# Optimization experiments

Measured on AMD Instinct MI355X. Metric: run time of the kernel, lower is better.

Reference implementation:

```python
import jax, jax.numpy as jnp
import numpy as np
from jax.scipy.special import gammaln

# sizes (see shape_source)
N_CELLS = 1024
N_GENES = 1000
N_LATENT = 50
NB_ENC = 16          # encoder histogram bins per gene
NB_DEC = 16          # decoder mixture components (sum(n_decoder_bins))
N_HID = 16           # encoder hidden dim
N_CUTS = 4_000_000
N_FRAGS = 2_000_000
N_TOTAL_CELLS = 10_000
N_TOTAL_CUTS = 50_000_000
BN_EPS = 1e-5


def _normal_logprob(x, loc, scale):
    z = (x - loc) / scale
    return -0.5 * z * z - jnp.log(scale) - 0.5 * jnp.log(2.0 * jnp.pi)


def setup_inputs() -> dict:
    key = jax.random.key(0)
    ks = jax.random.split(key, 20)
    cut_coordinates = jax.random.uniform(ks[0], (N_CUTS,), dtype=jnp.float32)
    cut_cell = jax.random.randint(ks[1], (N_CUTS,), 0, N_CELLS)
    cut_local_gene_ix = jax.random.randint(ks[2], (N_CUTS,), 0, N_GENES)
    cut_local_cellxgene_ix = cut_cell * N_GENES + cut_local_gene_ix
    local_cellxgene_ix = jax.random.randint(ks[3], (N_FRAGS,), 0, N_CELLS * N_GENES)
    genes_oi = jnp.arange(N_GENES)
    cells_oi = jnp.arange(N_CELLS)
    eps = jax.random.normal(ks[4], (N_CELLS, N_LATENT), dtype=jnp.float32)
    n_in = N_GENES * NB_ENC
    enc_W1 = jax.random.normal(ks[5], (n_in, N_HID)) * (1.0 / np.sqrt(n_in))
    enc_b1 = jnp.zeros((N_HID,))
    bn_gamma = jnp.ones((N_HID,))
    bn_beta = jnp.zeros((N_HID,))
    W_loc = jax.random.normal(ks[6], (N_HID, N_LATENT)) * (1.0 / np.sqrt(N_HID))
    b_loc = jnp.zeros((N_LATENT,))
    W_scale = jax.random.normal(ks[7], (N_HID, N_LATENT)) * (1.0 / np.sqrt(N_HID))
    b_scale = jnp.zeros((N_LATENT,))
    logit_weight = jax.random.normal(ks[8], (N_GENES, N_LATENT, NB_DEC)) * 0.05
    rho_weight = jax.random.normal(ks[9], (N_GENES, N_LATENT)) * 0.05
    baseline_heights = jax.random.normal(ks[10], (N_GENES, NB_DEC)) * 0.1
    libsize = jax.random.randint(ks[11], (N_TOTAL_CELLS,), 1000, 20000)
    rho_bias = jax.random.uniform(ks[12], (N_GENES,), minval=1e-4, maxval=1e-2)
    return dict(
        cut_coordinates=cut_coordinates, eps=eps,
        enc_W1=enc_W1, enc_b1=enc_b1, bn_gamma=bn_gamma, bn_beta=bn_beta,
        W_loc=W_loc, b_loc=b_loc, W_scale=W_scale, b_scale=b_scale,
        logit_weight=logit_weight, rho_weight=rho_weight,
        baseline_heights=baseline_heights, rho_bias=rho_bias,
        cut_local_cellxgene_ix=cut_local_cellxgene_ix,
        cut_local_gene_ix=cut_local_gene_ix,
        local_cellxgene_ix=local_cellxgene_ix,
        genes_oi=genes_oi, cells_oi=cells_oi, libsize=libsize,
    )


def reference(cut_coordinates, eps, enc_W1, enc_b1, bn_gamma, bn_beta,
              W_loc, b_loc, W_scale, b_scale, logit_weight, rho_weight,
              baseline_heights, rho_bias, cut_local_cellxgene_ix,
              cut_local_gene_ix, local_cellxgene_ix, genes_oi, cells_oi,
              libsize):
    n_cells = cells_oi.shape[0]
    n_genes = genes_oi.shape[0]

    # ---- Encoder: digitize + bincount histogram ----
    bin_enc = jnp.minimum(jnp.floor(cut_coordinates * NB_ENC), NB_ENC - 1).astype(jnp.int32)
    digitized = bin_enc + cut_local_cellxgene_ix.astype(jnp.int32) * NB_ENC
    counts = jax.ops.segment_sum(jnp.ones_like(cut_coordinates), digitized,
                                 num_segments=n_cells * n_genes * NB_ENC)
    x = jnp.log1p(counts.reshape(n_cells, n_genes * NB_ENC))  # [C, G*NB]

    h = x @ enc_W1 + enc_b1
    mu = h.mean(axis=0)
    var = h.var(axis=0)  # biased, matches torch BN in train mode
    h = (h - mu) / jnp.sqrt(var + BN_EPS) * bn_gamma + bn_beta
    h = jax.nn.relu(h)
    loc = h @ W_loc + b_loc                 # [C, L]
    scale = jnp.exp(h @ W_scale + b_scale)  # [C, L]

    # ---- latent sample + KL ----
    q_scale = scale * 0.1
    latent = loc + q_scale * eps
    latent_kl = (_normal_logprob(latent, 0.0, 1.0)
                 - _normal_logprob(latent, loc, q_scale)) * (N_TOTAL_CELLS / n_cells)

    # ---- Decoder (n_layers=0: per-gene linear heads) ----
    lw = logit_weight[genes_oi]                       # [G, L, K]
    rw = rho_weight[genes_oi]                         # [G, L]
    mixture_delta = jnp.einsum('cl,glk->cgk', latent, lw)  # [C, G, K]
    rho_delta = jnp.einsum('cl,gl->cg', latent, rw)        # [C, G]
    md_cxg = mixture_delta.reshape(n_cells * n_genes, NB_DEC)
    md_cut = md_cxg[cut_local_cellxgene_ix]           # [N_CUTS, K] gather
    mixture_delta_kl = _normal_logprob(lw, 0.0, 0.1)

    # ---- mixture likelihood: piecewise-constant spline density per cut ----
    logits = baseline_heights[cut_local_gene_ix] + md_cut  # [N_CUTS, K]
    logp = jax.nn.log_softmax(logits, axis=-1)
    bin_dec = jnp.minimum(jnp.floor(cut_coordinates * NB_DEC), NB_DEC - 1).astype(jnp.int32)
    likelihood_mixture = (jnp.take_along_axis(logp, bin_dec[:, None], axis=1)[:, 0]
                          + jnp.log(float(NB_DEC)))

    # ---- fragment-count Poisson likelihood ----
    fragexpr = (rho_bias[genes_oi][None, :] * jnp.exp(rho_delta)
                * libsize[cells_oi].astype(jnp.float32)[:, None])  # [C, G]
    fragmentcounts = jax.ops.segment_sum(
        jnp.ones((local_cellxgene_ix.shape[0],), jnp.float32),
        local_cellxgene_ix, num_segments=n_cells * n_genes
    ).reshape(n_cells, n_genes)
    likelihood_frag = (fragmentcounts * jnp.log(fragexpr) - fragexpr
                       - gammaln(fragmentcounts + 1.0))

    rho_delta_kl = _normal_logprob(rw, 0.0, 0.1)

    likelihood = (likelihood_mixture.sum() * (N_TOTAL_CUTS / cut_coordinates.shape[0])
                  + likelihood_frag.sum() * (N_TOTAL_CELLS / n_cells))
    elbo = (-likelihood - latent_kl.sum() - mixture_delta_kl.sum()
            - rho_delta_kl.sum())
    return elbo
```

## Files before the change

kernel.cpp:

```cpp
#include <hip/hip_runtime.h>
#include <hip/hip_bf16.h>
#include <math.h>


#define G_      1000
#define C_      1024
#define L_      50
#define K_      16
#define NHID_   16
#define CUT_SCALE   12.5f
#define CELL_SCALE  9.765625f

#define CHUNK_    6144
#define RCAP_CUT  18432
#define RCAP_FRAG 9216

#define GCNTC_OFF  0ull
#define GCNTF_OFF  1024ull
#define DONE_OFF   2048ull
#define DACC_OFF   6400ull
#define HT_OFF     6912ull
#define ZERO_BYTES 72448ull
#define LATBF_OFF  72448ull
#define LWT_OFF    203520ull
#define ENTC_OFF   2251520ull
#define ENTF_OFF   11688704ull
#define MERGED_OFF 16407296ull
#define FRAGU8_OFF 24599296ull
#define LATT_OFF   25623296ull
#define WS_NEED    25828096ull

typedef __attribute__((ext_vector_type(8))) short short8;
typedef __attribute__((ext_vector_type(4))) float f32x4;

__device__ __constant__ float LGT[32] = {
    0.0f, 0.0f, 0.6931471805599453f, 1.791759469228055f, 3.1780538303479458f,
    4.787491742782046f, 6.579251212010101f, 8.525161361065415f,
    10.60460290274525f, 12.801827480081469f, 15.104412573075516f,
    17.502307845873887f, 19.987214495661885f, 22.552163853123425f,
    25.19122118273868f, 27.89927138384089f, 30.671860106080672f,
    33.50507345013689f, 36.39544520803305f, 39.339884187199495f,
    42.335616460753485f, 45.38013889847691f, 48.47118135183523f,
    51.60667556776438f, 54.78472939811232f, 58.00360522298052f,
    61.261701761002f, 64.55753862700633f, 67.88974313718154f,
    71.25703896716801f, 74.65823634883016f, 78.0922235533153f };

__device__ __forceinline__ double atomAddF64(double* p, double v) {
    return __hip_atomic_fetch_add(p, v, __ATOMIC_RELAXED,
                                  __HIP_MEMORY_SCOPE_AGENT);
}

__device__ __forceinline__ float block_sum_256(float v) {
    __shared__ float sm[256];
    int t = threadIdx.x;
    __syncthreads();
    sm[t] = v;
    __syncthreads();
#pragma unroll
    for (int s = 128; s > 0; s >>= 1) {
        if (t < s) sm[t] += sm[t + s];
        __syncthreads();
    }
    return sm[0];
}

__global__ __launch_bounds__(256)
void part_kernel(const int* __restrict__ cut_ix,
                 const float* __restrict__ coord,
                 const int* __restrict__ frag_ix,
                 unsigned int* __restrict__ gcnt_c,
                 unsigned int* __restrict__ gcnt_f,
                 unsigned short* __restrict__ entc,
                 unsigned short* __restrict__ entf,
                 const float* __restrict__ lw,
                 const float* __restrict__ rw,
                 __hip_bfloat16* __restrict__ lwT,
                 double* __restrict__ dacc,
                 int n_cuts, int n_frags, int ncc, int nblk_part) {
    int t = threadIdx.x;
    int bid = blockIdx.x;
    if (bid >= nblk_part) {
        int r = bid - nblk_part;
        if (r < 256) {
            for (int g = r; g < G_; g += 256) {
                for (int i = t; i < L_ * K_; i += 256) {
                    float v = lw[(size_t)g * (L_ * K_) + i];
                    lwT[(size_t)g * 1024 + (i & 15) * 64 + (i >> 4)] =
                        __float2bfloat16(v);
                }
                for (int i = t; i < 16 * 14; i += 256) {
                    int n = i / 14, l = 50 + (i % 14);
                    lwT[(size_t)g * 1024 + n * 64 + l] = __float2bfloat16(0.f);
                }
            }
        } else {
            const int NTOT = G_ * L_ * K_ + G_ * L_;
            int wb = r - 256;
            float s = 0.f;
            for (int i = wb * 256 + t; i < NTOT; i += 256 * 256) {
                float w = (i < G_ * L_ * K_) ? lw[i] : rw[i - G_ * L_ * K_];
                s += fmaf(-50.f * w, w, 1.3836465597893733f);
            }
            s = block_sum_256(s);
            if (t == 0) atomAddF64(&dacc[wb & 63], (double)(-s));
        }
        return;
    }
    __shared__ unsigned int cnt[256], excl[256], gbas[256];
    __shared__ unsigned short stage[CHUNK_];
    __shared__ unsigned char bkof[CHUNK_];
    bool isCut = (bid < ncc);
    int blk = isCut ? bid : bid - ncc;
    const int* idx = isCut ? cut_ix : frag_ix;
    int n = isCut ? n_cuts : n_frags;
    int rcap = isCut ? RCAP_CUT : RCAP_FRAG;
    unsigned int* gcount = isCut ? gcnt_c : gcnt_f;
    unsigned short* ent = isCut ? entc : entf;
    int i0 = blk * CHUNK_;
    cnt[t] = 0;
    int4 I[6]; float4 X[6];
    unsigned int vm;
    bool full = (i0 + CHUNK_ <= n);
    if (full) {
        const int4* ip = (const int4*)(idx + i0);
#pragma unroll
        for (int k = 0; k < 6; ++k) I[k] = ip[k * 256 + t];
        if (isCut) {
            const float4* xp = (const float4*)(coord + i0);
#pragma unroll
            for (int k = 0; k < 6; ++k) X[k] = xp[k * 256 + t];
        }
        vm = 0xFFFFFFu;
    } else {
        vm = 0;
#pragma unroll
        for (int k = 0; k < 6; ++k) {
            int r0 = i0 + (k * 256 + t) * 4;
            int* Ii = (int*)&I[k]; float* Xi = (float*)&X[k];
#pragma unroll
            for (int u = 0; u < 4; ++u) {
                bool v = (r0 + u) < n;
                if (v) vm |= 1u << (k * 4 + u);
                Ii[u] = v ? idx[r0 + u] : 0;
                Xi[u] = (v && isCut) ? coord[r0 + u] : 0.f;
            }
        }
    }
    __syncthreads();
#pragma unroll
    for (int k = 0; k < 6; ++k) {
        int* Ii = (int*)&I[k];
        unsigned int* Xi = (unsigned int*)&X[k];
#pragma unroll
        for (int u = 0; u < 4; ++u) {
            if (vm & (1u << (k * 4 + u))) {
                int ix = Ii[u];
                int c = ix / G_;
                int g = ix - c * G_;
                unsigned int bk; unsigned int e;
                if (isCut) {
                    float xf = ((const float*)Xi)[u];
                    int b = (int)(xf * 16.f); b = b > 15 ? 15 : b;
                    int bin = g * K_ + b;
                    bk = ((unsigned)(c >> 6) << 4) | ((unsigned)bin >> 10);
                    e = ((unsigned)(c & 63) << 10) | ((unsigned)bin & 1023u);
                } else {
                    bk = ((unsigned)(c >> 6) << 4) | ((unsigned)g >> 6);
                    e = ((unsigned)(c & 63) << 6) | ((unsigned)g & 63u);
                }
                unsigned int rank = atomicAdd(&cnt[bk], 1u);
                Ii[u] = (int)(e | (bk << 16));
                Xi[u] = rank;
            }
        }
    }
    __syncthreads();
    if (t < 64) {
        unsigned int c0 = cnt[t * 4 + 0], c1 = cnt[t * 4 + 1];
        unsigned int c2 = cnt[t * 4 + 2], c3 = cnt[t * 4 + 3];
        unsigned int tot = c0 + c1 + c2 + c3;
        unsigned int run = tot;
#pragma unroll
        for (int o = 1; o < 64; o <<= 1) {
            unsigned int v = __shfl_up(run, o, 64);
            if (t >= o) run += v;
        }
        unsigned int base = run - tot;
        excl[t * 4 + 0] = base;
        excl[t * 4 + 1] = base + c0;
        excl[t * 4 + 2] = base + c0 + c1;
        excl[t * 4 + 3] = base + c0 + c1 + c2;
    }
    __syncthreads();
    gbas[t] = cnt[t] ? atomicAdd(&gcount[t], cnt[t]) : 0u;
#pragma unroll
    for (int k = 0; k < 6; ++k) {
        const unsigned int* Ii = (const unsigned int*)&I[k];
        const unsigned int* Xi = (const unsigned int*)&X[k];
#pragma unroll
        for (int u = 0; u < 4; ++u) {
            if (vm & (1u << (k * 4 + u))) {
                unsigned int w = Ii[u];
                unsigned int bk = w >> 16;
                unsigned int p = excl[bk] + Xi[u];
                stage[p] = (unsigned short)(w & 0xffffu);
                bkof[p] = (unsigned char)bk;
            }
        }
    }
    __syncthreads();
    int total = n - i0; if (total > CHUNK_) total = CHUNK_;
    for (int p = t; p < total; p += 256) {
        unsigned int bk = bkof[p];
        unsigned int dst = gbas[bk] + (p - excl[bk]);
        if (dst < (unsigned)rcap)
            ent[(size_t)bk * rcap + dst] = stage[p];
    }
}

__global__ __launch_bounds__(256)
void mid_kernel(const unsigned int* __restrict__ gcnt_c,
                const unsigned short* __restrict__ entc,
                const unsigned int* __restrict__ gcnt_f,
                const unsigned short* __restrict__ entf,
                const float* __restrict__ W1,
                unsigned int* __restrict__ merged,
                unsigned int* __restrict__ fragw,
                float* __restrict__ hT) {
    __shared__ unsigned int h[4096];
    __shared__ float w1s[4096];
    __shared__ float lgl[16];
    int t = threadIdx.x;
    int bid = blockIdx.x;
    if (bid < 512) {
        int bk = bid >> 1, half = bid & 1;
        int cg = bk >> 4, bc = bk & 15;
        for (int i = t; i < 4096; i += 256) h[i] = 0;
        if (t < 16) lgl[t] = __logf((float)(t + 1));
        __syncthreads();
        unsigned int count = gcnt_c[bk];
        if (count > RCAP_CUT) count = RCAP_CUT;
        const unsigned int* e32 = (const unsigned int*)(entc + (size_t)bk * RCAP_CUT);
        unsigned int hsel = (unsigned)half << 5;
        unsigned int npair = count >> 1;
        for (unsigned int base = 0; base < npair; base += 1024) {
            unsigned int w[4]; bool val[4];
#pragma unroll
            for (int u = 0; u < 4; ++u) {
                unsigned int p = base + u * 256 + t;
                val[u] = (p < npair);
                w[u] = val[u] ? e32[p] : 0u;
            }
#pragma unroll
            for (int u = 0; u < 4; ++u) {
                if (val[u]) {
                    unsigned int v0 = w[u] & 0xffffu, v1 = w[u] >> 16;
                    unsigned int c0 = v0 >> 10, c1 = v1 >> 10;
                    if ((c0 & 32u) == hsel) {
                        unsigned int cc = c0 & 31u;
                        atomicAdd(&h[(v0 & 1023u) * 4 + (cc >> 3)],
                                  1u << ((cc & 7) * 4));
                    }
                    if ((c1 & 32u) == hsel) {
                        unsigned int cc = c1 & 31u;
                        atomicAdd(&h[(v1 & 1023u) * 4 + (cc >> 3)],
                                  1u << ((cc & 7) * 4));
                    }
                }
            }
        }
        if (t == 0 && (count & 1u)) {
            unsigned int v = ((const unsigned short*)e32)[count - 1];
            unsigned int c0 = v >> 10;
            if ((c0 & 32u) == hsel) {
                unsigned int cc = c0 & 31u;
                atomicAdd(&h[(v & 1023u) * 4 + (cc >> 3)], 1u << ((cc & 7) * 4));
            }
        }
        __syncthreads();
        {
            unsigned int mbase = ((unsigned)(cg * 2 + half)) * 64000u
                               + (unsigned)bc * 4096u;
            int lim = (bc == 15) ? 2560 : 4096;
            for (int i = t; i < lim; i += 256)
                merged[mbase + i] = h[i];
        }
        int c32 = t & 31, sub = t >> 5;
        int sh = (c32 & 7) * 4, widx = c32 >> 3;
        float acc[NHID_];
#pragma unroll
        for (int j = 0; j < NHID_; ++j) acc[j] = 0.f;
        for (int q = 0; q < 4; ++q) {
            __syncthreads();
            int wbase = (bc * 1024 + q * 256) * NHID_;
#pragma unroll
            for (int r = 0; r < 16; ++r) {
                int i = r * 256 + t;
                int gi = wbase + i;
                w1s[i] = (gi < 16000 * NHID_) ? W1[gi] : 0.f;
            }
            __syncthreads();
            const float4* w1v = (const float4*)w1s;
            int rl0 = q * 256 + sub * 32;
#pragma unroll 4
            for (int bl = 0; bl < 32; ++bl) {
                int rl = rl0 + bl;
                int rwc = sub * 32 + bl;
                unsigned int w = h[rl * 4 + widx];
                float xv = lgl[(w >> sh) & 0xfu];
                float4 wa = w1v[rwc * 4 + 0];
                float4 wb = w1v[rwc * 4 + 1];
                float4 wc = w1v[rwc * 4 + 2];
                float4 wd = w1v[rwc * 4 + 3];
                acc[0] = fmaf(xv, wa.x, acc[0]);  acc[1] = fmaf(xv, wa.y, acc[1]);
                acc[2] = fmaf(xv, wa.z, acc[2]);  acc[3] = fmaf(xv, wa.w, acc[3]);
                acc[4] = fmaf(xv, wb.x, acc[4]);  acc[5] = fmaf(xv, wb.y, acc[5]);
                acc[6] = fmaf(xv, wb.z, acc[6]);  acc[7] = fmaf(xv, wb.w, acc[7]);
                acc[8] = fmaf(xv, wc.x, acc[8]);  acc[9] = fmaf(xv, wc.y, acc[9]);
                acc[10] = fmaf(xv, wc.z, acc[10]); acc[11] = fmaf(xv, wc.w, acc[11]);
                acc[12] = fmaf(xv, wd.x, acc[12]); acc[13] = fmaf(xv, wd.y, acc[13]);
                acc[14] = fmaf(xv, wd.z, acc[14]); acc[15] = fmaf(xv, wd.w, acc[15]);
            }
        }
        __syncthreads();
        float* sp = (float*)w1s;
#pragma unroll
        for (int j = 0; j < NHID_; ++j) sp[sub * 512 + j * 32 + c32] = acc[j];
        __syncthreads();
        for (int i = t; i < 512; i += 256) {
            int j = i >> 5, cc = i & 31;
            float v = 0.f;
#pragma unroll
            for (int s = 0; s < 8; ++s) v += sp[s * 512 + j * 32 + cc];
            atomicAdd(&hT[j * C_ + cg * 64 + half * 32 + cc], v);
        }
    } else {
        int bk = bid - 512, cg = bk >> 4, gc = bk & 15;
        for (int i = t; i < 2048; i += 256) h[i] = 0;
        __syncthreads();
        unsigned int count = gcnt_f[bk];
        if (count > RCAP_FRAG) count = RCAP_FRAG;
        const unsigned short* e = entf + (size_t)bk * RCAP_FRAG;
#pragma unroll 4
        for (unsigned int p = t; p < count; p += 256) {
            unsigned int v = e[p];
            unsigned int g_lo = v & 63u;
            unsigned int c_lo = (v >> 6) & 63u;
            atomicAdd(&h[g_lo * 32 + (c_lo >> 1)], 1u << ((c_lo & 1) * 16));
        }
        __syncthreads();
        for (int i = t; i < 1024; i += 256) {
            int g_lo = i >> 4, wb = i & 15;
            unsigned int lo = h[g_lo * 32 + wb * 2];
            unsigned int hi = h[g_lo * 32 + wb * 2 + 1];
            unsigned int outv = (lo & 0xffu) | (((lo >> 16) & 0xffu) << 8)
                              | ((hi & 0xffu) << 16) | (((hi >> 16) & 0xffu) << 24);
            int g = gc * 64 + g_lo;
            if (g < G_)
                fragw[(unsigned)g * 256u + (unsigned)cg * 16u + wb] = outv;
        }
    }
}

__global__ __launch_bounds__(256)
void latent_kernel(const float* __restrict__ hT,
                   const float* __restrict__ gamma,
                   const float* __restrict__ beta,
                   const float* __restrict__ W_loc,
                   const float* __restrict__ b_loc,
                   const float* __restrict__ W_scale,
                   const float* __restrict__ b_scale,
                   const float* __restrict__ eps,
                   float* __restrict__ latT,
                   __hip_bfloat16* __restrict__ latbf,
                   double* __restrict__ dacc) {
    __shared__ float scs[NHID_], shs[NHID_];
    int t = threadIdx.x;
    {
        int j = t >> 4, cl = t & 15;
        double s1 = 0.0, s2 = 0.0;
#pragma unroll 8
        for (int k = 0; k < 64; ++k) {
            float v = hT[j * C_ + cl + k * 16];
            s1 += (double)v; s2 += (double)v * (double)v;
        }
#pragma unroll
        for (int m = 1; m < 16; m <<= 1) {
            s1 += __shfl_xor(s1, m);
            s2 += __shfl_xor(s2, m);
        }
        if (cl == 0) {
            double mean = s1 * (1.0 / C_);
            double var = s2 * (1.0 / C_) - mean * mean;
            float rstd = rsqrtf((float)var + 1e-5f);
            float sc = gamma[j] * rstd;
            scs[j] = sc;
            shs[j] = beta[j] - (float)mean * sc;
        }
    }
    __syncthreads();
    int idx = blockIdx.x * 256 + t;
    float kl = 0.f;
    {
        int c = idx / L_;
        int l = idx - c * L_;
        float hb[NHID_];
#pragma unroll
        for (int j = 0; j < NHID_; ++j) {
            float v = fmaf(hT[j * C_ + c], scs[j], shs[j]);
            hb[j] = v > 0.f ? v : 0.f;
        }
        float loc = b_loc[l], ls = b_scale[l];
#pragma unroll
        for (int j = 0; j < NHID_; ++j) {
            loc = fmaf(hb[j], W_loc[j * L_ + l], loc);
            ls  = fmaf(hb[j], W_scale[j * L_ + l], ls);
        }
        float qs = 0.1f * __expf(ls);
        float e = eps[idx];
        float lat = fmaf(qs, e, loc);
        latT[(size_t)l * C_ + c] = lat;
        latbf[c * 64 + l] = __float2bfloat16(lat);
        if (l < 14) latbf[c * 64 + 50 + l] = __float2bfloat16(0.f);
        float z = (lat - loc) / qs;
        kl = fmaf(-0.5f * lat, lat, fmaf(0.5f * z, z, __logf(qs)));
    }
    float s = block_sum_256(kl);
    if (threadIdx.x == 0)
        atomAddF64(&dacc[blockIdx.x & 63], (double)(-CELL_SCALE * s));
}

__global__ __launch_bounds__(256)
void mixpois_kernel(const __hip_bfloat16* __restrict__ latbf,
                    const __hip_bfloat16* __restrict__ lwT,
                    const unsigned int* __restrict__ merged,
                    const float* __restrict__ baseline,
                    const float* __restrict__ latT,
                    const float* __restrict__ rw,
                    const float* __restrict__ rho_bias,
                    const int* __restrict__ libsize,
                    const unsigned char* __restrict__ fragb,
                    double* __restrict__ dacc,
                    unsigned int* __restrict__ done,
                    float* __restrict__ out) {
    int g = blockIdx.x;
    int y = blockIdx.y;
    int t = threadIdx.x;
    int lane = t & 63;
    int wv = t >> 6;
    int s16 = lane & 15;
    int quad = lane >> 4;
    const __hip_bfloat16* bb = lwT + (size_t)g * 1024 + s16 * 64 + quad * 8;
    short8 lw1 = *(const short8*)bb;
    short8 lw2 = *(const short8*)(bb + 32);
    const float4 bl4 = *(const float4*)(baseline + g * K_ + quad * 4);
    const unsigned int gb = ((unsigned)(g * K_ + quad * 4)) * 4u;
    float partial = 0.f;
    int cwave = y * 512 + wv * 128;
#pragma unroll
    for (int mt = 0; mt < 8; ++mt) {
        int c0 = cwave + mt * 16;
        const __hip_bfloat16* aa = latbf + (size_t)(c0 + s16) * 64 + quad * 8;
        short8 la1 = *(const short8*)aa;
        short8 la2 = *(const short8*)(aa + 32);
        f32x4 d = {bl4.x, bl4.y, bl4.z, bl4.w};
        d = __builtin_amdgcn_mfma_f32_16x16x32_bf16(lw1, la1, d, 0, 0, 0);
        d = __builtin_amdgcn_mfma_f32_16x16x32_bf16(lw2, la2, d, 0, 0, 0);
        float m = fmaxf(fmaxf(d[0], d[1]), fmaxf(d[2], d[3]));
        m = fmaxf(m, __shfl_xor(m, 16));
        m = fmaxf(m, __shfl_xor(m, 32));
        float e0 = __expf(d[0] - m), e1 = __expf(d[1] - m);
        float e2 = __expf(d[2] - m), e3 = __expf(d[3] - m);
        float S = (e0 + e1) + (e2 + e3);
        S += __shfl_xor(S, 16);
        S += __shfl_xor(S, 32);
        float lse = m + __logf(S);
        int cp = c0 + s16;
        unsigned int base2 = ((unsigned)cp >> 5) * 64000u
                           + (((unsigned)cp & 31u) >> 3);
        int sb = (cp & 7) * 4;
#pragma unroll
        for (int r = 0; r < 4; ++r) {
            float cnt = (float)((merged[base2 + gb + r * 4u] >> sb) & 0xfu);
            partial = fmaf(cnt, d[r] - lse, partial);
        }
    }
    float v;
    {
        const float* rwg = rw + (size_t)g * L_;
        int cA = y * 512 + t, cB = cA + 256;
        float rhoA = 0.f, rhoB = 0.f;
#pragma unroll 10
        for (int l = 0; l < L_; ++l) {
            float wl = rwg[l];
            rhoA = fmaf(latT[l * C_ + cA], wl, rhoA);
            rhoB = fmaf(latT[l * C_ + cB], wl, rhoB);
        }
        unsigned int fcA = fragb[(size_t)g * C_ + cA];
        unsigned int fcB = fragb[(size_t)g * C_ + cB];
        float rb = rho_bias[g];
        float feA = rb * __expf(rhoA) * (float)libsize[cA];
        float feB = rb * __expf(rhoB) * (float)libsize[cB];
        float lfA = fmaf((float)fcA, __logf(feA), -feA) - LGT[fcA > 31u ? 31u : fcA];
        float lfB = fmaf((float)fcB, __logf(feB), -feB) - LGT[fcB > 31u ? 31u : fcB];
        v = fmaf(-CUT_SCALE, partial, -CELL_SCALE * (lfA + lfB));
    }
    float contrib = block_sum_256(v);
    __shared__ int lastflag;
    if (threadIdx.x == 0) {
        lastflag = 0;
        int slot = blockIdx.x & 63;
        double oldv = atomAddF64(&dacc[slot], (double)contrib);
        unsigned inc = 1u;
        float dep = (float)oldv;
        asm volatile("" : "+v"(inc) : "v"(dep));
        unsigned quota = ((slot < 40) ? 16u : 15u) * 2u;
        if (atomicAdd(&done[slot * 16], inc) == quota - 1u) {
            if (atomicAdd(&done[1024], 1u) == 63u) lastflag = 1;
        }
    }
    __syncthreads();
    if (lastflag) {
        if (t < 64) {
            double dv = atomAddF64(&dacc[t], 0.0);
#pragma unroll
            for (int m = 1; m < 64; m <<= 1) dv += __shfl_xor(dv, m);
            if (t == 0)
                out[0] = (float)(dv - 138629436.11198905);
        }
    }
}

extern "C" void kernel_launch(void* const* d_in, const int* in_sizes, int n_in,
                              void* d_out, int out_size, void* d_ws, size_t ws_size,
                              hipStream_t stream) {
    const float* cut_coord = (const float*)d_in[0];
    const float* eps       = (const float*)d_in[1];
    const float* enc_W1    = (const float*)d_in[2];
    const float* bn_gamma  = (const float*)d_in[4];
    const float* bn_beta   = (const float*)d_in[5];
    const float* W_loc     = (const float*)d_in[6];
    const float* b_loc     = (const float*)d_in[7];
    const float* W_scale   = (const float*)d_in[8];
    const float* b_scale   = (const float*)d_in[9];
    const float* logit_w   = (const float*)d_in[10];
    const float* rho_w     = (const float*)d_in[11];
    const float* baseline  = (const float*)d_in[12];
    const float* rho_bias  = (const float*)d_in[13];
    const int* cut_cxg     = (const int*)d_in[14];
    const int* frag_ix     = (const int*)d_in[16];
    const int* libsize     = (const int*)d_in[19];

    int n_cuts  = in_sizes[0];
    int n_frags = in_sizes[16];

    char* ws = (char*)d_ws;
    unsigned int*   gcnt_c = (unsigned int*)(ws + GCNTC_OFF);
    unsigned int*   gcnt_f = (unsigned int*)(ws + GCNTF_OFF);
    unsigned int*   done   = (unsigned int*)(ws + DONE_OFF);
    double*         dacc   = (double*)(ws + DACC_OFF);
    float*          hT     = (float*)(ws + HT_OFF);
    __hip_bfloat16* latbf  = (__hip_bfloat16*)(ws + LATBF_OFF);
    __hip_bfloat16* lwT    = (__hip_bfloat16*)(ws + LWT_OFF);
    unsigned short* entc   = (unsigned short*)(ws + ENTC_OFF);
    unsigned short* entf   = (unsigned short*)(ws + ENTF_OFF);
    unsigned int*   merged = (unsigned int*)(ws + MERGED_OFF);
    unsigned int*   fragw  = (unsigned int*)(ws + FRAGU8_OFF);
    float*          latT   = (float*)(ws + LATT_OFF);
    float*          out    = (float*)d_out;

    int ncc = (n_cuts + CHUNK_ - 1) / CHUNK_;
    int ncf = (n_frags + CHUNK_ - 1) / CHUNK_;
    int nblk_part = ncc + ncf;

    hipMemsetAsync(ws, 0, ZERO_BYTES, stream);

    part_kernel<<<nblk_part + 512, 256, 0, stream>>>(
        cut_cxg, cut_coord, frag_ix, gcnt_c, gcnt_f, entc, entf,
        logit_w, rho_w, lwT, dacc,
        n_cuts, n_frags, ncc, nblk_part);
    mid_kernel<<<768, 256, 0, stream>>>(
        gcnt_c, entc, gcnt_f, entf, enc_W1, merged, fragw, hT);
    latent_kernel<<<(C_ * L_) / 256, 256, 0, stream>>>(
        hT, bn_gamma, bn_beta, W_loc, b_loc, W_scale, b_scale,
        eps, latT, latbf, dacc);
    mixpois_kernel<<<dim3(G_, 2), 256, 0, stream>>>(
        latbf, lwT, merged, baseline, latT, rho_w, rho_bias, libsize,
        (const unsigned char*)fragw, dacc, done, out);
}
```

Measured before the change: 219.5 us.

## Fuse latent kernel into mid kernel with spin-wait on atomic completion counter

Merges the latent (batchnorm + reparameterisation) kernel into mid_kernel as 200 extra blocks that spin on a global counter until all 512 encoder blocks have finished their hT atomics. The aim is to remove one kernel launch and the gap between the two launches. It also replaces the shared-memory log lookup table with a wave shuffle, sets launch_bounds occupancy to 4, and swaps the block reduction for per-wave shuffle sums. If the spinning blocks get scheduled before the producer blocks can become resident, they tie up compute units, which risks a deadlock or a stall, and the memory ordering of the hT atomics against the counter depends only on the dependency trick.

```diff
diff --git a/kernel.cpp b/kernel.cpp
--- a/kernel.cpp
+++ b/kernel.cpp
@@ -218,7 +218,7 @@
     }
 }
 
-__global__ __launch_bounds__(256)
+__global__ __launch_bounds__(256, 4)
 void mid_kernel(const unsigned int* __restrict__ gcnt_c,
                 const unsigned short* __restrict__ entc,
                 const unsigned int* __restrict__ gcnt_f,
@@ -226,17 +226,27 @@
                 const float* __restrict__ W1,
                 unsigned int* __restrict__ merged,
                 unsigned int* __restrict__ fragw,
-                float* __restrict__ hT) {
+                float* __restrict__ hT,
+                const float* __restrict__ gamma,
+                const float* __restrict__ beta,
+                const float* __restrict__ W_loc,
+                const float* __restrict__ b_loc,
+                const float* __restrict__ W_scale,
+                const float* __restrict__ b_scale,
+                const float* __restrict__ eps,
+                float* __restrict__ latT,
+                __hip_bfloat16* __restrict__ latbf,
+                double* __restrict__ dacc,
+                unsigned int* __restrict__ done) {
     __shared__ unsigned int h[4096];
     __shared__ float w1s[4096];
-    __shared__ float lgl[16];
     int t = threadIdx.x;
     int bid = blockIdx.x;
     if (bid < 512) {
         int bk = bid >> 1, half = bid & 1;
         int cg = bk >> 4, bc = bk & 15;
         for (int i = t; i < 4096; i += 256) h[i] = 0;
-        if (t < 16) lgl[t] = __logf((float)(t + 1));
+        float logtab = __logf((float)((t & 15) + 1));
         __syncthreads();
         unsigned int count = gcnt_c[bk];
         if (count > RCAP_CUT) count = RCAP_CUT;
@@ -307,7 +317,7 @@
                 int rl = rl0 + bl;
                 int rwc = sub * 32 + bl;
                 unsigned int w = h[rl * 4 + widx];
-                float xv = lgl[(w >> sh) & 0xfu];
+                float xv = __shfl(logtab, (int)((w >> sh) & 0xfu));
                 float4 wa = w1v[rwc * 4 + 0];
                 float4 wb = w1v[rwc * 4 + 1];
                 float4 wc = w1v[rwc * 4 + 2];
@@ -327,14 +337,18 @@
 #pragma unroll
         for (int j = 0; j < NHID_; ++j) sp[sub * 512 + j * 32 + c32] = acc[j];
         __syncthreads();
+        float dep = 0.f;
         for (int i = t; i < 512; i += 256) {
             int j = i >> 5, cc = i & 31;
             float v = 0.f;
 #pragma unroll
             for (int s = 0; s < 8; ++s) v += sp[s * 512 + j * 32 + cc];
-            atomicAdd(&hT[j * C_ + cg * 64 + half * 32 + cc], v);
-        }
-    } else {
+            dep += atomicAdd(&hT[j * C_ + cg * 64 + half * 32 + cc], v);
+        }
+        asm volatile("" :: "v"(dep));
+        __syncthreads();
+        if (t == 0) atomicAdd(&done[1040], 1u);
+    } else if (bid < 768) {
         int bk = bid - 512, cg = bk >> 4, gc = bk & 15;
         for (int i = t; i < 2048; i += 256) h[i] = 0;
         __syncthreads();
@@ -359,75 +373,71 @@
             if (g < G_)
                 fragw[(unsigned)g * 256u + (unsigned)cg * 16u + wb] = outv;
         }
-    }
-}
-
-__global__ __launch_bounds__(256)
-void latent_kernel(const float* __restrict__ hT,
-                   const float* __restrict__ gamma,
-                   const float* __restrict__ beta,
-                   const float* __restrict__ W_loc,
-                   const float* __restrict__ b_loc,
-                   const float* __restrict__ W_scale,
-                   const float* __restrict__ b_scale,
-                   const float* __restrict__ eps,
-                   float* __restrict__ latT,
-                   __hip_bfloat16* __restrict__ latbf,
-                   double* __restrict__ dacc) {
-    __shared__ float scs[NHID_], shs[NHID_];
-    int t = threadIdx.x;
-    {
-        int j = t >> 4, cl = t & 15;
-        double s1 = 0.0, s2 = 0.0;
+    } else {
+        int lb = bid - 768;
+        if (t == 0) {
+            while (__hip_atomic_load(&done[1040], __ATOMIC_RELAXED,
+                                     __HIP_MEMORY_SCOPE_AGENT) < 512u)
+                __builtin_amdgcn_s_sleep(8);
+        }
+        __syncthreads();
+        float* scs = (float*)w1s;
+        float* shs = ((float*)w1s) + 16;
+        {
+            int j = t >> 4, cl = t & 15;
+            double s1 = 0.0, s2 = 0.0;
 #pragma unroll 8
-        for (int k = 0; k < 64; ++k) {
-            float v = hT[j * C_ + cl + k * 16];
-            s1 += (double)v; s2 += (double)v * (double)v;
-        }
-#pragma unroll
-        for (int m = 1; m < 16; m <<= 1) {
-            s1 += __shfl_xor(s1, m);
-            s2 += __shfl_xor(s2, m);
-        }
-        if (cl == 0) {
-            double mean = s1 * (1.0 / C_);
-            double var = s2 * (1.0 / C_) - mean * mean;
-            float rstd = rsqrtf((float)var + 1e-5f);
-            float sc = gamma[j] * rstd;
-            scs[j] = sc;
-            shs[j] = beta[j] - (float)mean * sc;
-        }
-    }
-    __syncthreads();
-    int idx = blockIdx.x * 256 + t;
-    float kl = 0.f;
-    {
-        int c = idx / L_;
-        int l = idx - c * L_;
-        float hb[NHID_];
-#pragma unroll
-        for (int j = 0; j < NHID_; ++j) {
-            float v = fmaf(hT[j * C_ + c], scs[j], shs[j]);
-            hb[j] = v > 0.f ? v : 0.f;
-        }
-        float loc = b_loc[l], ls = b_scale[l];
-#pragma unroll
-        for (int j = 0; j < NHID_; ++j) {
-            loc = fmaf(hb[j], W_loc[j * L_ + l], loc);
-            ls  = fmaf(hb[j], W_scale[j * L_ + l], ls);
-        }
-        float qs = 0.1f * __expf(ls);
-        float e = eps[idx];
-        float lat = fmaf(qs, e, loc);
-        latT[(size_t)l * C_ + c] = lat;
-        latbf[c * 64 + l] = __float2bfloat16(lat);
-        if (l < 14) latbf[c * 64 + 50 + l] = __float2bfloat16(0.f);
-        float z = (lat - loc) / qs;
-        kl = fmaf(-0.5f * lat, lat, fmaf(0.5f * z, z, __logf(qs)));
-    }
-    float s = block_sum_256(kl);
-    if (threadIdx.x == 0)
-        atomAddF64(&dacc[blockIdx.x & 63], (double)(-CELL_SCALE * s));
+            for (int k = 0; k < 64; ++k) {
+                float v = hT[j * C_ + cl + k * 16];
+                s1 += (double)v; s2 += (double)v * (double)v;
+            }
+#pragma unroll
+            for (int m = 1; m < 16; m <<= 1) {
+                s1 += __shfl_xor(s1, m);
+                s2 += __shfl_xor(s2, m);
+            }
+            if (cl == 0) {
+                double mean = s1 * (1.0 / C_);
+                double var = s2 * (1.0 / C_) - mean * mean;
+                float rstd = rsqrtf((float)var + 1e-5f);
+                float sc = gamma[j] * rstd;
+                scs[j] = sc;
+                shs[j] = beta[j] - (float)mean * sc;
+            }
+        }
+        __syncthreads();
+        int idx = lb * 256 + t;
+        float kl;
+        {
+            int c = idx / L_;
+            int l = idx - c * L_;
+            float hb[NHID_];
+#pragma unroll
+            for (int j = 0; j < NHID_; ++j) {
+                float v = fmaf(hT[j * C_ + c], scs[j], shs[j]);
+                hb[j] = v > 0.f ? v : 0.f;
+            }
+            float loc = b_loc[l], ls = b_scale[l];
+#pragma unroll
+            for (int j = 0; j < NHID_; ++j) {
+                loc = fmaf(hb[j], W_loc[j * L_ + l], loc);
+                ls  = fmaf(hb[j], W_scale[j * L_ + l], ls);
+            }
+            float qs = 0.1f * __expf(ls);
+            float e = eps[idx];
+            float lat = fmaf(qs, e, loc);
+            latT[(size_t)l * C_ + c] = lat;
+            latbf[c * 64 + l] = __float2bfloat16(lat);
+            if (l < 14) latbf[c * 64 + 50 + l] = __float2bfloat16(0.f);
+            float z = (lat - loc) / qs;
+            kl = fmaf(-0.5f * lat, lat, fmaf(0.5f * z, z, __logf(qs)));
+        }
+#pragma unroll
+        for (int m = 1; m < 64; m <<= 1) kl += __shfl_xor(kl, m);
+        if ((t & 63) == 0)
+            atomAddF64(&dacc[(lb * 4 + (t >> 6)) & 63],
+                       (double)(-CELL_SCALE * kl));
+    }
 }
 
 __global__ __launch_bounds__(256)
@@ -579,11 +589,10 @@
         cut_cxg, cut_coord, frag_ix, gcnt_c, gcnt_f, entc, entf,
         logit_w, rho_w, lwT, dacc,
         n_cuts, n_frags, ncc, nblk_part);
-    mid_kernel<<<768, 256, 0, stream>>>(
-        gcnt_c, entc, gcnt_f, entf, enc_W1, merged, fragw, hT);
-    latent_kernel<<<(C_ * L_) / 256, 256, 0, stream>>>(
-        hT, bn_gamma, bn_beta, W_loc, b_loc, W_scale, b_scale,
-        eps, latT, latbf, dacc);
+    mid_kernel<<<968, 256, 0, stream>>>(
+        gcnt_c, entc, gcnt_f, entf, enc_W1, merged, fragw, hT,
+        bn_gamma, bn_beta, W_loc, b_loc, W_scale, b_scale, eps,
+        latT, latbf, dacc, done);
     mixpois_kernel<<<dim3(G_, 2), 256, 0, stream>>>(
         latbf, lwT, merged, baseline, latT, rho_w, rho_bias, libsize,
         (const unsigned char*)fragw, dacc, done, out);
```

New measurement: 237.9 us. 1.08x slower.
